# Kernel optimization log

Measured on AMD Instinct MI355X. Metric: run time of the kernel, lower is better.

## Reference

```python
import jax, jax.numpy as jnp
import numpy as np

DIM = 512
HEADS = 16
KS = 5  # side_dwconv


def setup_inputs() -> dict:
    key = jax.random.key(0)
    ks = jax.random.split(key, 6)
    B, H, W = 8, 32, 32
    x = jax.random.normal(ks[0], (B, H, W, DIM), dtype=jnp.float32)
    # qkv linear (no bias): torch Linear weight [3C, C]
    w_qkv = jax.random.normal(ks[1], (3 * DIM, DIM), dtype=jnp.float32) * (1.0 / np.sqrt(DIM))
    # output projection
    w_proj = jax.random.normal(ks[2], (DIM, DIM), dtype=jnp.float32) * (1.0 / np.sqrt(DIM))
    b_proj = jax.random.normal(ks[3], (DIM,), dtype=jnp.float32) * 0.01
    # depthwise conv kernel: torch Conv2d(groups=dim) weight [C, 1, k, k]
    w_lepe = jax.random.normal(ks[4], (DIM, 1, KS, KS), dtype=jnp.float32) * (1.0 / KS)
    b_lepe = jax.random.normal(ks[5], (DIM,), dtype=jnp.float32) * 0.01
    return {"x": x, "w_qkv": w_qkv, "w_proj": w_proj, "b_proj": b_proj,
            "w_lepe": w_lepe, "b_lepe": b_lepe}


def _depthwise_conv(x_nchw, w, b):
    # x: [B, C, H, W], w: [C, 1, k, k] (OIHW with feature_group_count=C)
    out = jax.lax.conv_general_dilated(
        x_nchw, w,
        window_strides=(1, 1),
        padding=[(KS // 2, KS // 2), (KS // 2, KS // 2)],
        dimension_numbers=("NCHW", "OIHW", "NCHW"),
        feature_group_count=x_nchw.shape[1],
    )
    return out + b[None, :, None, None]


def reference(x, w_qkv, w_proj, b_proj, w_lepe, b_lepe):
    B, H, W, C = x.shape
    N = H * W
    hd = C // HEADS
    scale = hd ** (-0.5)

    xt = x.reshape(B, N, C)  # n (h w) c

    qkv = xt @ w_qkv.T  # [B, N, 3C]
    qkv = qkv.reshape(B, N, 3, HEADS, hd).transpose(2, 0, 3, 1, 4)  # [3, B, h, N, d]
    q, k, v = qkv[0], qkv[1], qkv[2]

    # LePE depthwise conv positional encoding
    lepe = _depthwise_conv(xt.reshape(B, H, W, C).transpose(0, 3, 1, 2), w_lepe, b_lepe)
    lepe = lepe.transpose(0, 2, 3, 1).reshape(B, N, C)

    attn = jnp.einsum("bhnd,bhmd->bhnm", q, k) * scale
    attn = jax.nn.softmax(attn, axis=-1)
    out = jnp.einsum("bhnm,bhmd->bhnd", attn, v)
    out = out.transpose(0, 2, 1, 3).reshape(B, N, C)

    out = out + lepe
    out = out @ w_proj.T + b_proj
    return out.reshape(B, H, W, C)
```

## Files before the change

kernel.cpp:

```cpp
#include <hip/hip_runtime.h>
#include <hip/hip_bf16.h>

typedef unsigned int u32;
typedef unsigned short u16;
typedef __attribute__((ext_vector_type(8))) short bfrag;
typedef __attribute__((ext_vector_type(4))) float ffrag;
typedef __attribute__((ext_vector_type(4))) u32 u32x4;

__device__ __forceinline__ float bf2f(u16 h) { u32 v = ((u32)h) << 16; return __builtin_bit_cast(float, v); }
__device__ __forceinline__ u16 f2bf_bits(float f) {
  u32 x = __builtin_bit_cast(u32, f);
  x += 0x7FFFu + ((x >> 16) & 1u);
  return (u16)(x >> 16);
}
__device__ __forceinline__ u32 pack2f(float a, float b) {
  __hip_bfloat162 h = __float22bfloat162_rn(float2{a, b});
  u32 r;
  __builtin_memcpy(&r, &h, 4);
  return r;
}
__device__ __forceinline__ float fast_exp2(float x) {
#if __has_builtin(__builtin_amdgcn_exp2f)
  return __builtin_amdgcn_exp2f(x);
#else
  return __expf(x * 0.6931471805599453f);
#endif
}

__global__ __launch_bounds__(256) void qkv_gemm(const u16* __restrict__ Xb,
                                                const u16* __restrict__ Wqb,
                                                u16* __restrict__ qb,
                                                u16* __restrict__ kb,
                                                u16* __restrict__ vb) {
  __shared__ u16 As[128][40];
  __shared__ u16 Bs[128][40];
  const int tid = threadIdx.x;
  const int lane = tid & 63;
  const int w = tid >> 6;
  const int wr = w >> 1, wc = w & 1;
  const int lrow = lane & 15, quad = lane >> 4;
  const int bm0 = blockIdx.x * 128;
  const int bn0 = blockIdx.y * 128;
  const int lr = tid >> 1;
  const int lc = (tid & 1) * 16;

  ffrag acc[4][4];
#pragma unroll
  for (int i = 0; i < 4; i++)
#pragma unroll
    for (int j = 0; j < 4; j++) acc[i][j] = (ffrag){0.f, 0.f, 0.f, 0.f};

  const u16* arow = Xb + (bm0 + lr) * 512 + lc;
  const u16* brow = Wqb + (bn0 + lr) * 512 + lc;
  uint4 a0 = ((const uint4*)arow)[0], a1 = ((const uint4*)arow)[1];
  uint4 b0 = ((const uint4*)brow)[0], b1 = ((const uint4*)brow)[1];

  for (int k0 = 0; k0 < 512; k0 += 32) {
    __syncthreads();
    *(uint4*)(&As[lr][lc])     = a0;
    *(uint4*)(&As[lr][lc + 8]) = a1;
    *(uint4*)(&Bs[lr][lc])     = b0;
    *(uint4*)(&Bs[lr][lc + 8]) = b1;
    __syncthreads();
    if (k0 + 32 < 512) {
      const uint4* apn = (const uint4*)(arow + k0 + 32);
      const uint4* bpn = (const uint4*)(brow + k0 + 32);
      a0 = apn[0]; a1 = apn[1];
      b0 = bpn[0]; b1 = bpn[1];
    }
    bfrag af[4], bf[4];
#pragma unroll
    for (int i = 0; i < 4; i++) af[i] = *(const bfrag*)(&As[wr * 64 + i * 16 + lrow][quad * 8]);
#pragma unroll
    for (int j = 0; j < 4; j++) bf[j] = *(const bfrag*)(&Bs[wc * 64 + j * 16 + lrow][quad * 8]);
#pragma unroll
    for (int i = 0; i < 4; i++)
#pragma unroll
      for (int j = 0; j < 4; j++)
        acc[i][j] = __builtin_amdgcn_mfma_f32_16x16x32_bf16(af[i], bf[j], acc[i][j], 0, 0, 0);
  }

#pragma unroll
  for (int i = 0; i < 4; i++)
#pragma unroll
    for (int j = 0; j < 4; j++) {
      int jj = bn0 + wc * 64 + j * 16 + lrow;
      int which = jj >> 9, rem = jj & 511;
      int h = rem >> 5, d = rem & 31;
      u16* dst = (which == 0) ? qb : (which == 1) ? kb : vb;
#pragma unroll
      for (int r = 0; r < 4; r++) {
        int m = bm0 + wr * 64 + i * 16 + quad * 4 + r;
        int pair = ((m >> 10) << 4) + h;
        int n = m & 1023;
        dst[(pair * 1024 + n) * 32 + d] = f2bf_bits(acc[i][j][r]);
      }
    }
}

__global__ __launch_bounds__(256) void lepe_conv(const float* __restrict__ X,
                                                 const float* __restrict__ Wl,
                                                 const float* __restrict__ bl,
                                                 const float* __restrict__ Wq,
                                                 const float* __restrict__ Wp,
                                                 u16* __restrict__ out,
                                                 u16* __restrict__ xb,
                                                 u16* __restrict__ wqb,
                                                 u16* __restrict__ wpb) {
  if (blockIdx.z == 2) {
    const int t = (blockIdx.y * 32 + blockIdx.x) * 256 + threadIdx.x;
    const int NQ = 196608;
#pragma unroll
    for (int k = 0; k < 4; k++) {
      int idx = t + k * 65536;
      const float* src;
      u16* dst;
      int off;
      if (idx < NQ) { src = Wq; dst = wqb; off = idx; }
      else          { src = Wp; dst = wpb; off = idx - NQ; }
      float4 v = ((const float4*)src)[off];
      uint2 r;
      r.x = pack2f(v.x, v.y);
      r.y = pack2f(v.z, v.w);
      ((uint2*)dst)[off] = r;
    }
    return;
  }

  __shared__ float Wls[512 * 25];
  const int tid = threadIdx.x;
  const int c = tid * 2;
  const int y = blockIdx.x;
  const int b = blockIdx.y;
  const int x0 = blockIdx.z * 16;

  {
    const float2* src = (const float2*)Wl;
    float2* dst = (float2*)Wls;
#pragma unroll
    for (int i = 0; i < 25; i++) dst[tid + i * 256] = src[tid + i * 256];
  }
  __syncthreads();

  float w0[25], w1[25];
#pragma unroll
  for (int t = 0; t < 25; t++) {
    w0[t] = Wls[c * 25 + t];
    w1[t] = Wls[(c + 1) * 25 + t];
  }
  const float2 bias = *(const float2*)(bl + c);

  const float* rowp[5];
  bool rowv[5];
#pragma unroll
  for (int r = 0; r < 5; r++) {
    int yy = y + r - 2;
    rowv[r] = (yy >= 0) && (yy < 32);
    rowp[r] = X + ((b * 32 + (rowv[r] ? yy : 0)) * 32) * 512 + c;
  }

  float2 win[5][5];
#pragma unroll
  for (int rel = -2; rel <= 1; rel++) {
    const int slot = ((rel % 5) + 5) % 5;
    const int xcol = x0 + rel;
    const bool xv = (xcol >= 0) && (xcol < 32);
#pragma unroll
    for (int r = 0; r < 5; r++)
      win[r][slot] = (xv && rowv[r]) ? *(const float2*)(rowp[r] + xcol * 512)
                                     : float2{0.f, 0.f};
  }

#pragma unroll
  for (int xi = 0; xi < 16; xi++) {
    {
      const int slot = (xi + 2) % 5;
      const int xcol = x0 + xi + 2;
      const bool xv = (xcol < 32);
#pragma unroll
      for (int r = 0; r < 5; r++)
        win[r][slot] = (xv && rowv[r]) ? *(const float2*)(rowp[r] + xcol * 512)
                                       : float2{0.f, 0.f};
    }
    float a0 = bias.x, a1 = bias.y;
#pragma unroll
    for (int ky = 0; ky < 5; ky++)
#pragma unroll
      for (int kx = 0; kx < 5; kx++) {
        const int rel = xi - 2 + kx;
        const int slot = ((rel % 5) + 5) % 5;
        const float2 v = win[ky][slot];
        const int t = ky * 5 + kx;
        a0 = fmaf(v.x, w0[t], a0);
        a1 = fmaf(v.y, w1[t], a1);
      }
    const int sp = (b * 32 + y) * 32 + x0 + xi;
    *(u32*)(out + sp * 512 + c) = pack2f(a0, a1);
    const float2 ctr = win[2][xi % 5];
    *(u32*)(xb + sp * 512 + c) = pack2f(ctr.x, ctr.y);
  }
}

__global__ __launch_bounds__(512, 4) void attn_mfma(const u16* __restrict__ qb,
                                                    const u16* __restrict__ kb,
                                                    const u16* __restrict__ vb,
                                                    const u16* __restrict__ lp,
                                                    u16* __restrict__ ao) {
  __shared__ u32 Vt[32][132];
  const int tid = threadIdx.x, lane = tid & 63, w = tid >> 6;
  const int quad = lane >> 4, m16 = lane & 15;
  const int pair = blockIdx.x >> 2;
  const int quarter = blockIdx.x & 3;
  const int b = pair >> 4, h = pair & 15;

  const int wq0 = quarter * 256 + w * 32;
  bfrag qf[2];
#pragma unroll
  for (int i = 0; i < 2; i++) {
    int row = wq0 + i * 16 + m16;
    qf[i] = *(const bfrag*)(qb + (pair * 1024 + row) * 32 + quad * 8);
  }

  const float SC2 = 0.25503448540239605f;
  const float SHIFT2 = 11.541560327111707f;
  const u16* kbase = kb + pair * 32768;
  const u16* vbase = vb + pair * 32768;

  bfrag onesf;
#pragma unroll
  for (int e = 0; e < 8; e++) onesf[e] = (short)0x3F80;

  ffrag oacc[2][2], sacc[2];
#pragma unroll
  for (int i = 0; i < 2; i++) {
    oacc[i][0] = (ffrag){0.f, 0.f, 0.f, 0.f};
    oacc[i][1] = (ffrag){0.f, 0.f, 0.f, 0.f};
    sacc[i]    = (ffrag){0.f, 0.f, 0.f, 0.f};
  }

  const int pp = tid & 127;
  const int vq = tid >> 7;
  const int vg = pp >> 4, vt = pp & 15;
  const int jbase = vg * 32 + vt;
  uint4 svl = *(const uint4*)(vbase + jbase * 32 + vq * 8);
  uint4 svh = *(const uint4*)(vbase + (jbase + 16) * 32 + vq * 8);

  bfrag kf0n = *(const bfrag*)(kbase + (m16) * 32 + quad * 8);
  bfrag kf1n = *(const bfrag*)(kbase + (16 + m16) * 32 + quad * 8);

  for (int jc = 0; jc < 1024; jc += 256) {
    __syncthreads();
    {
      u32 lw[4] = {svl.x, svl.y, svl.z, svl.w};
      u32 hw[4] = {svh.x, svh.y, svh.z, svh.w};
#pragma unroll
      for (int e = 0; e < 4; e++) {
        int d0 = vq * 8 + e * 2;
        Vt[d0][pp]     = (lw[e] & 0xFFFFu) | (hw[e] << 16);
        Vt[d0 + 1][pp] = (lw[e] >> 16) | (hw[e] & 0xFFFF0000u);
      }
    }
    __syncthreads();
    if (jc + 256 < 1024) {
      int jlo = jc + 256 + jbase;
      svl = *(const uint4*)(vbase + jlo * 32 + vq * 8);
      svh = *(const uint4*)(vbase + (jlo + 16) * 32 + vq * 8);
    }

    for (int j0 = 0; j0 < 256; j0 += 32) {
      const int g0 = j0 >> 5;
      bfrag kf0 = kf0n, kf1 = kf1n;
      {
        const int jn = jc + j0 + 32;
        kf0n = *(const bfrag*)(kbase + (jn + m16) * 32 + quad * 8);
        kf1n = *(const bfrag*)(kbase + (jn + 16 + m16) * 32 + quad * 8);
      }
      bfrag vf0 = *(const bfrag*)(&Vt[m16][g0 * 16 + quad * 4]);
      bfrag vf1 = *(const bfrag*)(&Vt[16 + m16][g0 * 16 + quad * 4]);

      ffrag s[2][2];
      __builtin_amdgcn_s_setprio(1);
#pragma unroll
      for (int i = 0; i < 2; i++) {
        s[i][0] = __builtin_amdgcn_mfma_f32_16x16x32_bf16(kf0, qf[i], (ffrag){0.f,0.f,0.f,0.f}, 0, 0, 0);
        s[i][1] = __builtin_amdgcn_mfma_f32_16x16x32_bf16(kf1, qf[i], (ffrag){0.f,0.f,0.f,0.f}, 0, 0, 0);
      }
      __builtin_amdgcn_s_setprio(0);

      bfrag pa[2];
#pragma unroll
      for (int i = 0; i < 2; i++) {
        u32x4 paw;
#pragma unroll
        for (int r = 0; r < 4; r++) {
          float p0 = fast_exp2(fmaf(s[i][0][r], SC2, -SHIFT2));
          float p1 = fast_exp2(fmaf(s[i][1][r], SC2, -SHIFT2));
          paw[r] = pack2f(p0, p1);
        }
        pa[i] = __builtin_bit_cast(bfrag, paw);
      }

      __builtin_amdgcn_s_setprio(1);
#pragma unroll
      for (int i = 0; i < 2; i++) {
        sacc[i]    = __builtin_amdgcn_mfma_f32_16x16x32_bf16(pa[i], onesf, sacc[i], 0, 0, 0);
        oacc[i][0] = __builtin_amdgcn_mfma_f32_16x16x32_bf16(pa[i], vf0, oacc[i][0], 0, 0, 0);
        oacc[i][1] = __builtin_amdgcn_mfma_f32_16x16x32_bf16(pa[i], vf1, oacc[i][1], 0, 0, 0);
      }
      __builtin_amdgcn_s_setprio(0);
    }
  }

#pragma unroll
  for (int i = 0; i < 2; i++) {
    float inv[4];
#pragma unroll
    for (int r = 0; r < 4; r++) inv[r] = 1.0f / sacc[i][r];
#pragma unroll
    for (int jd = 0; jd < 2; jd++)
#pragma unroll
      for (int r = 0; r < 4; r++) {
        int row = wq0 + i * 16 + quad * 4 + r;
        int col = jd * 16 + m16;
        int o = (b * 1024 + row) * 512 + h * 32 + col;
        float val = fmaf(oacc[i][jd][r], inv[r], bf2f(lp[o]));
        ao[o] = f2bf_bits(val);
      }
  }
}

__global__ __launch_bounds__(256) void proj_gemm(const u16* __restrict__ Y,
                                                 const u16* __restrict__ Wpb,
                                                 const float* __restrict__ bp,
                                                 float* __restrict__ out) {
  __shared__ u16 As[128][40];
  __shared__ u16 Bs[64][40];
  const int tid = threadIdx.x;
  const int lane = tid & 63;
  const int w = tid >> 6;
  const int wr = w >> 1, wc = w & 1;
  const int lrow = lane & 15, quad = lane >> 4;
  const int bm0 = blockIdx.x * 128;
  const int bn0 = blockIdx.y * 64;
  const int lr = tid >> 1;
  const int lc = (tid & 1) * 16;
  const int br = tid >> 2;
  const int bc = (tid & 3) * 8;

  ffrag acc[4][2];
#pragma unroll
  for (int i = 0; i < 4; i++)
#pragma unroll
    for (int j = 0; j < 2; j++) acc[i][j] = (ffrag){0.f, 0.f, 0.f, 0.f};

  const u16* arow = Y + (bm0 + lr) * 512 + lc;
  const u16* brow = Wpb + (bn0 + br) * 512 + bc;
  uint4 a0 = ((const uint4*)arow)[0], a1 = ((const uint4*)arow)[1];
  uint4 b0 = *(const uint4*)brow;

  for (int k0 = 0; k0 < 512; k0 += 32) {
    __syncthreads();
    *(uint4*)(&As[lr][lc])     = a0;
    *(uint4*)(&As[lr][lc + 8]) = a1;
    *(uint4*)(&Bs[br][bc])     = b0;
    __syncthreads();
    if (k0 + 32 < 512) {
      const uint4* apn = (const uint4*)(arow + k0 + 32);
      a0 = apn[0]; a1 = apn[1];
      b0 = *(const uint4*)(brow + k0 + 32);
    }
    bfrag af[4], bf[2];
#pragma unroll
    for (int i = 0; i < 4; i++) af[i] = *(const bfrag*)(&As[wr * 64 + i * 16 + lrow][quad * 8]);
#pragma unroll
    for (int j = 0; j < 2; j++) bf[j] = *(const bfrag*)(&Bs[wc * 32 + j * 16 + lrow][quad * 8]);
#pragma unroll
    for (int i = 0; i < 4; i++)
#pragma unroll
      for (int j = 0; j < 2; j++)
        acc[i][j] = __builtin_amdgcn_mfma_f32_16x16x32_bf16(af[i], bf[j], acc[i][j], 0, 0, 0);
  }

#pragma unroll
  for (int i = 0; i < 4; i++)
#pragma unroll
    for (int j = 0; j < 2; j++) {
      int jj = bn0 + wc * 32 + j * 16 + lrow;
      float bias = bp[jj];
#pragma unroll
      for (int r = 0; r < 4; r++) {
        int m = bm0 + wr * 64 + i * 16 + quad * 4 + r;
        out[m * 512 + jj] = acc[i][j][r] + bias;
      }
    }
}

extern "C" void kernel_launch(void* const* d_in, const int* in_sizes, int n_in,
                              void* d_out, int out_size, void* d_ws, size_t ws_size,
                              hipStream_t stream) {
  const float* x      = (const float*)d_in[0];
  const float* w_qkv  = (const float*)d_in[1];
  const float* w_proj = (const float*)d_in[2];
  const float* b_proj = (const float*)d_in[3];
  const float* w_lepe = (const float*)d_in[4];
  const float* b_lepe = (const float*)d_in[5];
  float* out = (float*)d_out;

  char* ws = (char*)d_ws;
  const size_t SEG = 8388608;
  u16* qb  = (u16*)(ws + 0 * SEG);
  u16* kb  = (u16*)(ws + 1 * SEG);
  u16* vb  = (u16*)(ws + 2 * SEG);
  u16* ao  = (u16*)(ws + 3 * SEG);
  u16* lp  = (u16*)(ws + 4 * SEG);
  u16* xb  = (u16*)(ws + 5 * SEG);
  u16* wqb = (u16*)(ws + 6 * SEG);
  u16* wpb = (u16*)(ws + 6 * SEG + 1572864);

  hipLaunchKernelGGL(lepe_conv, dim3(32, 8, 3), dim3(256), 0, stream,
                     x, w_lepe, b_lepe, w_qkv, w_proj, lp, xb, wqb, wpb);
  hipLaunchKernelGGL(qkv_gemm, dim3(64, 12), dim3(256), 0, stream, xb, wqb, qb, kb, vb);
  hipLaunchKernelGGL(attn_mfma, dim3(512), dim3(512), 0, stream, qb, kb, vb, lp, ao);
  hipLaunchKernelGGL(proj_gemm, dim3(64, 8), dim3(256), 0, stream, ao, wpb, b_proj, out);
}
```

Baseline: 158.2 us.

## Use direct global-to-LDS loads with fragment-ordered LDS layout in GEMMs

Both the QKV and output-projection GEMMs now copy tiles from global memory straight into LDS with global_load_lds, instead of staging them through registers. The LDS tiles are rearranged so each 16x32 MFMA fragment sits contiguously in lane order, which makes the fragment reads conflict-free. This gives up the old register-prefetch pipelining: the load for each k-step is issued after the first barrier and waited on before compute, so global latency is no longer hidden behind the MFMA work.

```diff
diff --git a/kernel.cpp b/kernel.cpp
--- a/kernel.cpp
+++ b/kernel.cpp
@@ -27,13 +27,19 @@
 #endif
 }
 
+typedef const __attribute__((address_space(1))) void* gas_t;
+typedef __attribute__((address_space(3))) void* las_t;
+__device__ __forceinline__ void gload_lds16(const void* g, void* ldsbase) {
+  __builtin_amdgcn_global_load_lds((gas_t)g, (las_t)ldsbase, 16, 0, 0);
+}
+
 __global__ __launch_bounds__(256) void qkv_gemm(const u16* __restrict__ Xb,
                                                 const u16* __restrict__ Wqb,
                                                 u16* __restrict__ qb,
                                                 u16* __restrict__ kb,
                                                 u16* __restrict__ vb) {
-  __shared__ u16 As[128][40];
-  __shared__ u16 Bs[128][40];
+  __shared__ u16 As[8192];
+  __shared__ u16 Bs[8192];
   const int tid = threadIdx.x;
   const int lane = tid & 63;
   const int w = tid >> 6;
@@ -41,8 +47,6 @@
   const int lrow = lane & 15, quad = lane >> 4;
   const int bm0 = blockIdx.x * 128;
   const int bn0 = blockIdx.y * 128;
-  const int lr = tid >> 1;
-  const int lc = (tid & 1) * 16;
 
   ffrag acc[4][4];
 #pragma unroll
@@ -50,29 +54,27 @@
 #pragma unroll
     for (int j = 0; j < 4; j++) acc[i][j] = (ffrag){0.f, 0.f, 0.f, 0.f};
 
-  const u16* arow = Xb + (bm0 + lr) * 512 + lc;
-  const u16* brow = Wqb + (bn0 + lr) * 512 + lc;
-  uint4 a0 = ((const uint4*)arow)[0], a1 = ((const uint4*)arow)[1];
-  uint4 b0 = ((const uint4*)brow)[0], b1 = ((const uint4*)brow)[1];
+  const int ab0 = w * 2;
+  const int ab1 = w * 2 + 1;
+  const int arow0 = (ab0 >> 2) * 64 + (ab0 & 3) * 16 + lrow;
+  const int arow1 = (ab1 >> 2) * 64 + (ab1 & 3) * 16 + lrow;
+  const u16* gA0 = Xb + (bm0 + arow0) * 512 + quad * 8;
+  const u16* gA1 = Xb + (bm0 + arow1) * 512 + quad * 8;
+  const u16* gB0 = Wqb + (bn0 + arow0) * 512 + quad * 8;
+  const u16* gB1 = Wqb + (bn0 + arow1) * 512 + quad * 8;
 
   for (int k0 = 0; k0 < 512; k0 += 32) {
     __syncthreads();
-    *(uint4*)(&As[lr][lc])     = a0;
-    *(uint4*)(&As[lr][lc + 8]) = a1;
-    *(uint4*)(&Bs[lr][lc])     = b0;
-    *(uint4*)(&Bs[lr][lc + 8]) = b1;
-    __syncthreads();
-    if (k0 + 32 < 512) {
-      const uint4* apn = (const uint4*)(arow + k0 + 32);
-      const uint4* bpn = (const uint4*)(brow + k0 + 32);
-      a0 = apn[0]; a1 = apn[1];
-      b0 = bpn[0]; b1 = bpn[1];
-    }
+    gload_lds16(gA0 + k0, &As[ab0 * 512]);
+    gload_lds16(gA1 + k0, &As[ab1 * 512]);
+    gload_lds16(gB0 + k0, &Bs[ab0 * 512]);
+    gload_lds16(gB1 + k0, &Bs[ab1 * 512]);
+    __syncthreads();
     bfrag af[4], bf[4];
 #pragma unroll
-    for (int i = 0; i < 4; i++) af[i] = *(const bfrag*)(&As[wr * 64 + i * 16 + lrow][quad * 8]);
-#pragma unroll
-    for (int j = 0; j < 4; j++) bf[j] = *(const bfrag*)(&Bs[wc * 64 + j * 16 + lrow][quad * 8]);
+    for (int i = 0; i < 4; i++) af[i] = *(const bfrag*)(&As[(wr * 4 + i) * 512 + lane * 8]);
+#pragma unroll
+    for (int j = 0; j < 4; j++) bf[j] = *(const bfrag*)(&Bs[(wc * 4 + j) * 512 + lane * 8]);
 #pragma unroll
     for (int i = 0; i < 4; i++)
 #pragma unroll
@@ -333,8 +335,8 @@
                                                  const u16* __restrict__ Wpb,
                                                  const float* __restrict__ bp,
                                                  float* __restrict__ out) {
-  __shared__ u16 As[128][40];
-  __shared__ u16 Bs[64][40];
+  __shared__ u16 As[8192];
+  __shared__ u16 Bs[4096];
   const int tid = threadIdx.x;
   const int lane = tid & 63;
   const int w = tid >> 6;
@@ -342,10 +344,6 @@
   const int lrow = lane & 15, quad = lane >> 4;
   const int bm0 = blockIdx.x * 128;
   const int bn0 = blockIdx.y * 64;
-  const int lr = tid >> 1;
-  const int lc = (tid & 1) * 16;
-  const int br = tid >> 2;
-  const int bc = (tid & 3) * 8;
 
   ffrag acc[4][2];
 #pragma unroll
@@ -353,27 +351,24 @@
 #pragma unroll
     for (int j = 0; j < 2; j++) acc[i][j] = (ffrag){0.f, 0.f, 0.f, 0.f};
 
-  const u16* arow = Y + (bm0 + lr) * 512 + lc;
-  const u16* brow = Wpb + (bn0 + br) * 512 + bc;
-  uint4 a0 = ((const uint4*)arow)[0], a1 = ((const uint4*)arow)[1];
-  uint4 b0 = *(const uint4*)brow;
+  const int ab0 = w * 2, ab1 = w * 2 + 1;
+  const int arow0 = (ab0 >> 2) * 64 + (ab0 & 3) * 16 + lrow;
+  const int arow1 = (ab1 >> 2) * 64 + (ab1 & 3) * 16 + lrow;
+  const u16* gA0 = Y + (bm0 + arow0) * 512 + quad * 8;
+  const u16* gA1 = Y + (bm0 + arow1) * 512 + quad * 8;
+  const u16* gB0 = Wpb + (bn0 + w * 16 + lrow) * 512 + quad * 8;
 
   for (int k0 = 0; k0 < 512; k0 += 32) {
     __syncthreads();
-    *(uint4*)(&As[lr][lc])     = a0;
-    *(uint4*)(&As[lr][lc + 8]) = a1;
-    *(uint4*)(&Bs[br][bc])     = b0;
-    __syncthreads();
-    if (k0 + 32 < 512) {
-      const uint4* apn = (const uint4*)(arow + k0 + 32);
-      a0 = apn[0]; a1 = apn[1];
-      b0 = *(const uint4*)(brow + k0 + 32);
-    }
+    gload_lds16(gA0 + k0, &As[ab0 * 512]);
+    gload_lds16(gA1 + k0, &As[ab1 * 512]);
+    gload_lds16(gB0 + k0, &Bs[w * 512]);
+    __syncthreads();
     bfrag af[4], bf[2];
 #pragma unroll
-    for (int i = 0; i < 4; i++) af[i] = *(const bfrag*)(&As[wr * 64 + i * 16 + lrow][quad * 8]);
-#pragma unroll
-    for (int j = 0; j < 2; j++) bf[j] = *(const bfrag*)(&Bs[wc * 32 + j * 16 + lrow][quad * 8]);
+    for (int i = 0; i < 4; i++) af[i] = *(const bfrag*)(&As[(wr * 4 + i) * 512 + lane * 8]);
+#pragma unroll
+    for (int j = 0; j < 2; j++) bf[j] = *(const bfrag*)(&Bs[(wc * 2 + j) * 512 + lane * 8]);
 #pragma unroll
     for (int i = 0; i < 4; i++)
 #pragma unroll
```

Result: slower. 169.6 us (+7.2%).
